# Optimization experiments

Measured on AMD Instinct MI355X. Metric: run time of the kernel, lower is better.

Reference implementation:

```python
import jax, jax.numpy as jnp
import numpy as np

T, B, L, CTX, H = 512, 512, 16, 64, 128
STATE_DIM, SHOT, PID, DATA = 32, 12, 35, 23


def setup_inputs() -> dict:
    key = jax.random.key(0)
    ks = jax.random.split(key, 64)
    k = iter(ks)
    def rn(shape, s=0.1):
        return (jax.random.normal(next(k), shape) * s).astype(jnp.float32)
    xs = jax.random.normal(next(k), (T, B, DATA), jnp.float32)
    xs = xs.at[:, :, 12].set(jax.random.randint(next(k), (T, B), 0, SHOT).astype(jnp.float32))
    xs = xs.at[:, :, 17].set(jax.random.randint(next(k), (T, B), 0, PID).astype(jnp.float32))
    xs = xs.at[:, :, 20].set(jax.random.randint(next(k), (T, B), 0, SHOT).astype(jnp.float32))
    return dict(
        total_xs=jnp.zeros((1,), jnp.float32),
        xs=xs,
        ts=jnp.linspace(0.0, 2.0, T).astype(jnp.float32),
        noise_std=jnp.asarray(0.1, jnp.float32),
        z0_noise=jax.random.normal(next(k), (B, L), jnp.float32),
        bm_noise=jax.random.normal(next(k), (T - 1, B, L), jnp.float32),
        shot_emb=rn((SHOT, 8)), player_emb=rn((PID, 8)),
        gru_wih=rn((3 * H, STATE_DIM)), gru_whh=rn((3 * H, H)),
        gru_bih=rn((3 * H,)), gru_bhh=rn((3 * H,)),
        enc_w=rn((CTX, H)), enc_b=rn((CTX,)),
        qz0_w=rn((2 * L, CTX)), qz0_b=rn((2 * L,)),
        f_w1=rn((H, L + CTX)), f_b1=rn((H,)), f_w2=rn((H, H)), f_b2=rn((H,)),
        f_w3=rn((L, H)), f_b3=rn((L,)),
        h_w1=rn((H, L)), h_b1=rn((H,)), h_w2=rn((H, H)), h_b2=rn((H,)),
        h_w3=rn((L, H)), h_b3=rn((L,)),
        g_w1=rn((L, H)), g_b1=rn((L, H)), g_w2=rn((L, H)), g_b2=rn((L,)),
        proj_w=rn((STATE_DIM, L)), proj_b=rn((STATE_DIM,)),
        pz0_mean=jnp.zeros((1, L), jnp.float32), pz0_logstd=jnp.zeros((1, L), jnp.float32),
        act_w=rn((128, L)), act_b=rn((128,)),
        act_land_w=rn((2, 128)), act_shot_w=rn((SHOT, 128)), act_move_w=rn((2, 128)),
    )


def _forward(xs, noise_std, shot_emb, player_emb, gru_wih, gru_whh, gru_bih, gru_bhh,
             enc_w, enc_b, qz0_w, qz0_b,
             f_w1, f_b1, f_w2, f_b2, f_w3, f_b3,
             h_w1, h_b1, h_w2, h_b2, h_w3, h_b3,
             g_w1, g_b1, g_w2, g_b2,
             proj_w, proj_b, pz0_mean, pz0_logstd,
             act_w, act_b, act_land_w, act_shot_w, act_move_w,
             ts, z0_noise, bm_noise):
    # --- SDE_embed_and_transform: replace shot/player id cols with embeddings ---
    state = xs[:, :, :18]
    shot_ids = state[:, :, 12].astype(jnp.int32)
    pid_ids = state[:, :, 17].astype(jnp.int32)
    state_t = jnp.concatenate([state[:, :, :12], shot_emb[shot_ids],
                               state[:, :, 13:17], player_emb[pid_ids]], axis=-1)  # (T,B,32)
    xs_t = jnp.concatenate([state_t, xs[:, :, 18:]], axis=-1)  # (T,B,37)
    # --- Encoder: GRU over time-reversed states, linear head, flip back ---
    def gru_step(h, xt):
        gi = xt @ gru_wih.T + gru_bih
        gh = h @ gru_whh.T + gru_bhh
        ir, iz, inn = jnp.split(gi, 3, axis=-1)
        hr, hz, hn = jnp.split(gh, 3, axis=-1)
        r = jax.nn.sigmoid(ir + hr)
        zg = jax.nn.sigmoid(iz + hz)
        n = jnp.tanh(inn + r * hn)
        hnew = (1.0 - zg) * n + zg * h
        return hnew, hnew
    h0 = jnp.zeros((xs.shape[1], gru_whh.shape[1]), xs.dtype)
    _, hs = jax.lax.scan(gru_step, h0, state_t[::-1])
    ctx = (hs @ enc_w.T + enc_b)[::-1]  # (T,B,CTX)
    # --- posterior z0 ---
    qm, qls = jnp.split(ctx[0] @ qz0_w.T + qz0_b, 2, axis=1)
    z0 = qm + jnp.exp(qls) * z0_noise
    # --- Euler-Maruyama with logqp; searchsorted(right) -> ctx[min(i+1,T-1)] = ctx[i+1] ---
    dts = ts[1:] - ts[:-1]  # (T-1,)
    dW = jnp.sqrt(dts)[:, None, None] * bm_noise
    ctx_steps = ctx[1:]
    def mlp3(x, w1, b1, w2, b2, w3, b3):
        h1 = jax.nn.softplus(x @ w1.T + b1)
        h2 = jax.nn.softplus(h1 @ w2.T + b2)
        return h2 @ w3.T + b3
    def g_diag(y):  # (B,L): per-latent-dim scalar nets, batched over L
        hg = jax.nn.softplus(y[:, :, None] * g_w1[None] + g_b1[None])  # (B,L,H)
        return jax.nn.sigmoid(jnp.einsum('blh,lh->bl', hg, g_w2) + g_b2)
    def sde_step(z, inp):
        c, dw, dt = inp
        f_val = mlp3(jnp.concatenate([z, c], axis=1), f_w1, f_b1, f_w2, f_b2, f_w3, f_b3)
        h_val = mlp3(z, h_w1, h_b1, h_w2, h_b2, h_w3, h_b3)
        g_val = g_diag(z)
        u = (f_val - h_val) / g_val
        logr = 0.5 * jnp.sum(u * u, axis=1) * dt
        z_new = z + f_val * dt + g_val * dw
        return z_new, (z_new, logr)
    _, (z_tail, log_ratio) = jax.lax.scan(sde_step, z0, (ctx_steps, dW, dts))
    zs = jnp.concatenate([z0[None], z_tail], axis=0)  # (T,B,L)
    _xs = zs @ proj_w.T + proj_b  # (T,B,32)
    # --- action model losses ---
    a = jax.nn.relu(zs @ act_w.T + act_b)
    land = (a @ act_land_w.T).reshape(-1, 2)
    shot_logits = (a @ act_shot_w.T).reshape(-1, act_shot_w.shape[0])
    move = (a @ act_move_w.T).reshape(-1, 2)
    true_actions = xs_t[:, :, -5:]
    true_land = true_actions[:, :, :2].reshape(-1, 2)
    true_move = true_actions[:, :, 3:].reshape(-1, 2)
    true_shot = true_actions[:, :, 2].astype(jnp.int32).reshape(-1)
    land_loss = jnp.mean((land - true_land) ** 2)
    move_loss = jnp.mean((move - true_move) ** 2)
    logp = jax.nn.log_softmax(shot_logits, axis=-1)
    picked = jnp.take_along_axis(logp, true_shot[:, None], axis=1)[:, 0]
    mask = (true_shot != 0).astype(logp.dtype)  # CrossEntropy ignore_index=0
    shot_loss = -jnp.sum(picked * mask) / jnp.maximum(jnp.sum(mask), 1.0)
    # --- reconstruction log-likelihood ---
    xs_state = xs_t[:, :, :STATE_DIM]
    LOG2PI = 1.8378770664093453
    log_pxs = jnp.mean(jnp.sum(
        -0.5 * ((xs_state - _xs) / noise_std) ** 2 - jnp.log(noise_std) - 0.5 * LOG2PI,
        axis=(0, 2)))
    # --- KL(q(z0) || p(z0)) ---
    var_q = jnp.exp(2.0 * qls)
    var_p = jnp.exp(2.0 * pz0_logstd)
    kl = pz0_logstd - qls + (var_q + (qm - pz0_mean) ** 2) / (2.0 * var_p) - 0.5
    logqp0 = jnp.mean(jnp.sum(kl, axis=1))
    logqp_path = jnp.mean(jnp.sum(log_ratio, axis=0))
    return log_pxs, logqp0 + logqp_path + land_loss + shot_loss + move_loss


def reference(total_xs, xs, ts, noise_std, z0_noise, bm_noise, shot_emb, player_emb,
              gru_wih, gru_whh, gru_bih, gru_bhh, enc_w, enc_b, qz0_w, qz0_b,
              f_w1, f_b1, f_w2, f_b2, f_w3, f_b3, h_w1, h_b1, h_w2, h_b2, h_w3, h_b3,
              g_w1, g_b1, g_w2, g_b2, proj_w, proj_b, pz0_mean, pz0_logstd,
              act_w, act_b, act_land_w, act_shot_w, act_move_w):
    return _forward(xs, noise_std, shot_emb, player_emb, gru_wih, gru_whh, gru_bih, gru_bhh,
                    enc_w, enc_b, qz0_w, qz0_b,
                    f_w1, f_b1, f_w2, f_b2, f_w3, f_b3,
                    h_w1, h_b1, h_w2, h_b2, h_w3, h_b3,
                    g_w1, g_b1, g_w2, g_b2,
                    proj_w, proj_b, pz0_mean, pz0_logstd,
                    act_w, act_b, act_land_w, act_shot_w, act_move_w,
                    ts, z0_noise, bm_noise)
```

## Files before the change

### kernel.cpp

```cpp
#include <hip/hip_runtime.h>
#include <cstdint>

typedef _Float16 f16;
typedef _Float16 f16x2 __attribute__((ext_vector_type(2)));

#define T_STEPS 512
#define B_SZ 512
#define LOG2PI 1.8378770664093453f

__device__ __forceinline__ uint32_t packh2(float a, float b) {
  f16x2 v; v[0] = (f16)a; v[1] = (f16)b;
  return __builtin_bit_cast(uint32_t, v);
}

__device__ __forceinline__ float fdot2(uint32_t a, uint32_t b, float c) {
#if defined(__AMDGCN__) && __has_builtin(__builtin_amdgcn_fdot2)
  return __builtin_amdgcn_fdot2(__builtin_bit_cast(f16x2, a),
                                __builtin_bit_cast(f16x2, b), c, false);
#else
  f16x2 x = __builtin_bit_cast(f16x2, a), y = __builtin_bit_cast(f16x2, b);
  return c + (float)x[0] * (float)y[0] + (float)x[1] * (float)y[1];
#endif
}

#define DOT4(acc, w0, w1, w2, w3, v)                                     \
  do {                                                                   \
    acc = fdot2((w0), (v).x, acc); acc = fdot2((w1), (v).y, acc);        \
    acc = fdot2((w2), (v).z, acc); acc = fdot2((w3), (v).w, acc);        \
  } while (0)

__device__ __forceinline__ float sigmoidf_(float x) {
  return 1.0f / (1.0f + __expf(-x));
}
__device__ __forceinline__ float tanhf_(float x) {
  float ax = fabsf(x);
  float t = __expf(-2.0f * ax);
  float r = (1.0f - t) / (1.0f + t);
  return copysignf(r, x);
}
__device__ __forceinline__ float softplusf_(float x) {
  return fmaxf(x, 0.0f) + __logf(1.0f + __expf(-fabsf(x)));
}

__global__ __launch_bounds__(256) void k_embed(
    const float* __restrict__ xs, const float* __restrict__ shot_emb,
    const float* __restrict__ player_emb, f16* __restrict__ state_t,
    float* __restrict__ accums) {
  if (blockIdx.x == 0 && threadIdx.x < 16) accums[threadIdx.x] = 0.0f;
  size_t idx = (size_t)blockIdx.x * 256 + threadIdx.x;
  const float* xp = xs + idx * 23;
  f16* op = state_t + idx * 32;
  int sid = (int)xp[12];
  int pid = (int)xp[17];
#pragma unroll
  for (int i = 0; i < 12; ++i) op[i] = (f16)xp[i];
  const float* se = shot_emb + sid * 8;
#pragma unroll
  for (int i = 0; i < 8; ++i) op[12 + i] = (f16)se[i];
#pragma unroll
  for (int i = 0; i < 4; ++i) op[20 + i] = (f16)xp[13 + i];
  const float* pe = player_emb + pid * 8;
#pragma unroll
  for (int i = 0; i < 8; ++i) op[24 + i] = (f16)pe[i];
}

__global__ __launch_bounds__(448, 4) void k_gru(
    const f16* __restrict__ state_t, const float* __restrict__ wih,
    const float* __restrict__ whh, const float* __restrict__ bih,
    const float* __restrict__ bhh, const float* __restrict__ enc_w,
    const float* __restrict__ enc_b, const float* __restrict__ qz0_w,
    const float* __restrict__ qz0_b, const float* __restrict__ z0_noise,
    const float* __restrict__ pz0_mean, const float* __restrict__ pz0_logstd,
    f16* __restrict__ ctx, float* __restrict__ z0_out,
    float* __restrict__ accums) {
  __shared__ __align__(16) uint32_t s_x[16];
  __shared__ __align__(16) uint32_t s_h[64];
  __shared__ float s_gi[384], s_gh[384];
  __shared__ float s_ctx0[64];
  __shared__ float s_q[32];

  const int tid = threadIdx.x;
  const int bg = blockIdx.x;
  const uint32_t* stu = (const uint32_t*)state_t;

  uint32_t wA[64];
  uint32_t wB[16];
  float bi = 0.f, bh = 0.f, encbr = 0.f;

  if (tid < 384) {
    const float* whr = whh + (size_t)tid * 128;
#pragma unroll
    for (int i = 0; i < 64; ++i) wA[i] = packh2(whr[2 * i], whr[2 * i + 1]);
    const float* wxr = wih + (size_t)tid * 32;
#pragma unroll
    for (int i = 0; i < 16; ++i) wB[i] = packh2(wxr[2 * i], wxr[2 * i + 1]);
    bi = bih[tid];
    bh = bhh[tid];
  } else {
    int cc = tid - 384;
    const float* wer = enc_w + (size_t)cc * 128;
#pragma unroll
    for (int i = 0; i < 64; ++i) wA[i] = packh2(wer[2 * i], wer[2 * i + 1]);
    encbr = enc_b[cc];
  }

  if (tid < 64) s_h[tid] = 0u;
  if (tid < 4)
    *(uint4*)&s_x[tid * 4] =
        *(const uint4*)(stu + ((size_t)(T_STEPS - 1) * B_SZ + bg) * 16 + tid * 4);
  float h_old = 0.0f;
  __syncthreads();

  for (int t = T_STEPS - 1; t >= 0; --t) {
    uint4 xpref = make_uint4(0, 0, 0, 0);
    if (tid >= 128 && tid < 132 && t > 0)
      xpref = *(const uint4*)(stu + ((size_t)(t - 1) * B_SZ + bg) * 16 +
                              (tid - 128) * 4);
    if (tid < 384) {
      float ax0 = bi, ax1 = 0.f;
      const uint4* xq = (const uint4*)s_x;
#pragma unroll
      for (int j = 0; j < 4; ++j) {
        uint4 v = xq[j];
        if (j & 1) { DOT4(ax1, wB[4 * j], wB[4 * j + 1], wB[4 * j + 2], wB[4 * j + 3], v); }
        else       { DOT4(ax0, wB[4 * j], wB[4 * j + 1], wB[4 * j + 2], wB[4 * j + 3], v); }
      }
      float ah0 = bh, ah1 = 0.f;
      const uint4* hq = (const uint4*)s_h;
#pragma unroll
      for (int j = 0; j < 16; ++j) {
        uint4 v = hq[j];
        if (j & 1) { DOT4(ah1, wA[4 * j], wA[4 * j + 1], wA[4 * j + 2], wA[4 * j + 3], v); }
        else       { DOT4(ah0, wA[4 * j], wA[4 * j + 1], wA[4 * j + 2], wA[4 * j + 3], v); }
      }
      s_gi[tid] = ax0 + ax1;
      s_gh[tid] = ah0 + ah1;
    } else if (t < T_STEPS - 1) {
      int cc = tid - 384;
      float a0 = encbr, a1 = 0.f;
      const uint4* hq = (const uint4*)s_h;
#pragma unroll
      for (int j = 0; j < 16; ++j) {
        uint4 v = hq[j];
        if (j & 1) { DOT4(a1, wA[4 * j], wA[4 * j + 1], wA[4 * j + 2], wA[4 * j + 3], v); }
        else       { DOT4(a0, wA[4 * j], wA[4 * j + 1], wA[4 * j + 2], wA[4 * j + 3], v); }
      }
      ctx[((size_t)(t + 1) * B_SZ + bg) * 64 + cc] = (f16)(a0 + a1);
    }
    __syncthreads();
    if (tid < 128) {
      float r = sigmoidf_(s_gi[tid] + s_gh[tid]);
      float zg = sigmoidf_(s_gi[128 + tid] + s_gh[128 + tid]);
      float n = tanhf_(s_gi[256 + tid] + r * s_gh[256 + tid]);
      float hnew = (1.0f - zg) * n + zg * h_old;
      h_old = hnew;
      ((f16*)s_h)[tid] = (f16)hnew;
    } else if (tid >= 128 && tid < 132 && t > 0) {
      *(uint4*)&s_x[(tid - 128) * 4] = xpref;
    }
    __syncthreads();
  }

  if (tid >= 384) {
    int cc = tid - 384;
    float a0 = encbr, a1 = 0.f;
    const uint4* hq = (const uint4*)s_h;
#pragma unroll
    for (int j = 0; j < 16; ++j) {
      uint4 v = hq[j];
      if (j & 1) { DOT4(a1, wA[4 * j], wA[4 * j + 1], wA[4 * j + 2], wA[4 * j + 3], v); }
      else       { DOT4(a0, wA[4 * j], wA[4 * j + 1], wA[4 * j + 2], wA[4 * j + 3], v); }
    }
    float val = a0 + a1;
    ctx[(size_t)bg * 64 + cc] = (f16)val;
    s_ctx0[cc] = val;
  }
  __syncthreads();
  if (tid < 32) {
    float acc = qz0_b[tid];
#pragma unroll 8
    for (int k = 0; k < 64; ++k) acc += qz0_w[tid * 64 + k] * s_ctx0[k];
    s_q[tid] = acc;
  }
  __syncthreads();
  if (tid < 16) {
    float qm = s_q[tid], qls = s_q[16 + tid];
    float z0v = qm + __expf(qls) * z0_noise[bg * 16 + tid];
    z0_out[bg * 16 + tid] = z0v;
    float pm = pz0_mean[tid], pls = pz0_logstd[tid];
    float var_q = __expf(2.0f * qls);
    float var_p = __expf(2.0f * pls);
    float dm = qm - pm;
    float kl = pls - qls + (var_q + dm * dm) / (2.0f * var_p) - 0.5f;
    atomicAdd(&accums[5], kl);
  }
}

__global__ __launch_bounds__(256, 2) void k_sde(
    const f16* __restrict__ ctx, const float* __restrict__ z0_in,
    const float* __restrict__ ts, const float* __restrict__ bm_noise,
    const float* __restrict__ fw1, const float* __restrict__ fb1,
    const float* __restrict__ fw2, const float* __restrict__ fb2,
    const float* __restrict__ fw3, const float* __restrict__ fb3,
    const float* __restrict__ hw1, const float* __restrict__ hb1,
    const float* __restrict__ hw2, const float* __restrict__ hb2,
    const float* __restrict__ hw3, const float* __restrict__ hb3,
    const float* __restrict__ gw1, const float* __restrict__ gb1,
    const float* __restrict__ gw2, const float* __restrict__ gb2,
    f16* __restrict__ zs, float* __restrict__ accums) {
  __shared__ __align__(16) uint32_t s_x2[40];
  __shared__ __align__(16) uint32_t s_h1f[64];
  __shared__ __align__(16) uint32_t s_h1h[64];
  __shared__ __align__(16) uint32_t s_h2[2][64];
  __shared__ float s_zf[16];
  __shared__ __align__(16) float s_gp[128];
  __shared__ __align__(16) float s_p3[256];
  __shared__ float s_dts[T_STEPS];

  const int tid = threadIdx.x;
  const int bg = blockIdx.x;

  uint32_t uw[56];
  uint32_t wP2[64];
  uint32_t wP3[8];
  float bias1r = 0.f, bias2r = 0.f, gb2r = 0.f, fb3r = 0.f, hb3r = 0.f;

  if (tid < 128) {
    const float* w = fw1 + (size_t)tid * 80;
#pragma unroll
    for (int i = 0; i < 40; ++i) uw[i] = packh2(w[2 * i], w[2 * i + 1]);
    bias1r = fb1[tid];
  } else {
    int u = tid - 128;
    const float* w = hw1 + (size_t)u * 16;
#pragma unroll
    for (int i = 0; i < 8; ++i) uw[i] = packh2(w[2 * i], w[2 * i + 1]);
    bias1r = hb1[u];
    int l = u & 15, k8 = u >> 4;
#pragma unroll
    for (int i = 0; i < 16; ++i) {
      int h = k8 * 16 + i;
      uw[8 + i] = __builtin_bit_cast(uint32_t, gw1[l * 128 + h]);
      uw[24 + i] = __builtin_bit_cast(uint32_t, gb1[l * 128 + h]);
      uw[40 + i] = __builtin_bit_cast(uint32_t, gw2[l * 128 + h]);
    }
  }
  {
    int mlp = tid >> 7, u = tid & 127;
    const float* w = (mlp ? hw2 : fw2) + (size_t)u * 128;
#pragma unroll
    for (int i = 0; i < 64; ++i) wP2[i] = packh2(w[2 * i], w[2 * i + 1]);
    bias2r = (mlp ? hb2 : fb2)[u];
  }
  {
    int mlp = tid >> 7, o = tid & 15, k8 = (tid >> 4) & 7;
    const float* w = (mlp ? hw3 : fw3) + (size_t)o * 128 + k8 * 16;
#pragma unroll
    for (int i = 0; i < 8; ++i) wP3[i] = packh2(w[2 * i], w[2 * i + 1]);
  }
  if (tid < 16) {
    fb3r = fb3[tid];
    hb3r = hb3[tid];
    gb2r = gb2[tid];
  }
  for (int i = tid; i < T_STEPS - 1; i += 256) s_dts[i] = ts[i + 1] - ts[i];

  if (tid < 16) {
    float z = z0_in[bg * 16 + tid];
    s_zf[tid] = z;
    ((f16*)s_x2)[tid] = (f16)z;
    zs[(size_t)bg * 16 + tid] = (f16)z;
  }
  if (tid >= 16 && tid < 24) {
    int q = tid - 16;
    *(uint4*)&s_x2[8 + q * 4] =
        *(const uint4*)((const uint32_t*)ctx + ((size_t)1 * B_SZ + bg) * 32 + q * 4);
  }
  float path_acc = 0.0f;
  __syncthreads();

  for (int t = 0; t < T_STEPS - 1; ++t) {
    float bm_cur = 0.f;
    uint4 cpref = make_uint4(0, 0, 0, 0);
    if (tid < 16) bm_cur = bm_noise[((size_t)t * B_SZ + bg) * 16 + tid];
    if (tid >= 16 && tid < 24 && t <= T_STEPS - 3) {
      int q = tid - 16;
      cpref = *(const uint4*)((const uint32_t*)ctx +
                              ((size_t)(t + 2) * B_SZ + bg) * 32 + q * 4);
    }
    if (tid < 128) {
      float a0 = bias1r, a1 = 0.f;
      const uint4* xq = (const uint4*)s_x2;
#pragma unroll
      for (int j = 0; j < 10; ++j) {
        uint4 v = xq[j];
        if (j & 1) { DOT4(a1, uw[4 * j], uw[4 * j + 1], uw[4 * j + 2], uw[4 * j + 3], v); }
        else       { DOT4(a0, uw[4 * j], uw[4 * j + 1], uw[4 * j + 2], uw[4 * j + 3], v); }
      }
      ((f16*)s_h1f)[tid] = (f16)softplusf_(a0 + a1);
    } else {
      int u = tid - 128;
      const uint4* zq = (const uint4*)s_x2;
      float a0 = bias1r, a1 = 0.f;
      uint4 v0 = zq[0], v1 = zq[1];
      DOT4(a0, uw[0], uw[1], uw[2], uw[3], v0);
      DOT4(a1, uw[4], uw[5], uw[6], uw[7], v1);
      ((f16*)s_h1h)[u] = (f16)softplusf_(a0 + a1);
      int l = u & 15, k8 = u >> 4;
      float y = s_zf[l];
      float acc = 0.f;
#pragma unroll
      for (int i = 0; i < 16; ++i) {
        float pre = fmaf(y, __builtin_bit_cast(float, uw[8 + i]),
                         __builtin_bit_cast(float, uw[24 + i]));
        acc = fmaf(softplusf_(pre), __builtin_bit_cast(float, uw[40 + i]), acc);
      }
      s_gp[l * 8 + k8] = acc;
    }
    __syncthreads();
    {
      const uint4* hq = (const uint4*)((tid >> 7) ? s_h1h : s_h1f);
      float a0 = bias2r, a1 = 0.f, a2 = 0.f, a3 = 0.f;
#pragma unroll
      for (int j = 0; j < 16; j += 4) {
        uint4 v0 = hq[j], v1 = hq[j + 1], v2 = hq[j + 2], v3 = hq[j + 3];
        DOT4(a0, wP2[4 * j], wP2[4 * j + 1], wP2[4 * j + 2], wP2[4 * j + 3], v0);
        DOT4(a1, wP2[4 * j + 4], wP2[4 * j + 5], wP2[4 * j + 6], wP2[4 * j + 7], v1);
        DOT4(a2, wP2[4 * j + 8], wP2[4 * j + 9], wP2[4 * j + 10], wP2[4 * j + 11], v2);
        DOT4(a3, wP2[4 * j + 12], wP2[4 * j + 13], wP2[4 * j + 14], wP2[4 * j + 15], v3);
      }
      ((f16*)s_h2[tid >> 7])[tid & 127] = (f16)softplusf_((a0 + a1) + (a2 + a3));
    }
    __syncthreads();
    {
      int mlp = tid >> 7, o = tid & 15, k8 = (tid >> 4) & 7;
      const uint4* hq = (const uint4*)&s_h2[mlp][k8 * 8];
      uint4 v0 = hq[0], v1 = hq[1];
      float a0 = 0.f, a1 = 0.f;
      DOT4(a0, wP3[0], wP3[1], wP3[2], wP3[3], v0);
      DOT4(a1, wP3[4], wP3[5], wP3[6], wP3[7], v1);
      s_p3[(mlp * 16 + o) * 8 + k8] = a0 + a1;
    }
    __syncthreads();
    if (tid < 16) {
      int l = tid;
      const float4* fp = (const float4*)&s_p3[l * 8];
      const float4* hp = (const float4*)&s_p3[(16 + l) * 8];
      const float4* gp = (const float4*)&s_gp[l * 8];
      float4 f0 = fp[0], f1v = fp[1], h0 = hp[0], h1v = hp[1];
      float4 g0 = gp[0], g1 = gp[1];
      float fv = fb3r + ((f0.x + f0.y) + (f0.z + f0.w)) +
                 ((f1v.x + f1v.y) + (f1v.z + f1v.w));
      float hv = hb3r + ((h0.x + h0.y) + (h0.z + h0.w)) +
                 ((h1v.x + h1v.y) + (h1v.z + h1v.w));
      float gv = sigmoidf_(gb2r + ((g0.x + g0.y) + (g0.z + g0.w)) +
                           ((g1.x + g1.y) + (g1.z + g1.w)));
      float dt = s_dts[t];
      float u = (fv - hv) / gv;
      float lsum = u * u;
      lsum += __shfl_xor(lsum, 1);
      lsum += __shfl_xor(lsum, 2);
      lsum += __shfl_xor(lsum, 4);
      lsum += __shfl_xor(lsum, 8);
      if (l == 0) path_acc += 0.5f * lsum * dt;
      float zn = s_zf[l] + fv * dt + gv * (sqrtf(dt) * bm_cur);
      s_zf[l] = zn;
      ((f16*)s_x2)[l] = (f16)zn;
      zs[((size_t)(t + 1) * B_SZ + bg) * 16 + l] = (f16)zn;
    } else if (tid >= 16 && tid < 24 && t <= T_STEPS - 3) {
      int q = tid - 16;
      *(uint4*)&s_x2[8 + q * 4] = cpref;
    }
    __syncthreads();
  }
  if (tid == 0) atomicAdd(&accums[6], path_acc);
}

__global__ __launch_bounds__(256) void k_dec(
    const f16* __restrict__ zs, const f16* __restrict__ state_t,
    const float* __restrict__ xs, const float* __restrict__ proj_w,
    const float* __restrict__ proj_b, const float* __restrict__ act_w,
    const float* __restrict__ act_b, const float* __restrict__ land_w,
    const float* __restrict__ shot_w, const float* __restrict__ move_w,
    float* __restrict__ accums) {
  __shared__ __align__(16) uint32_t s_proj[32 * 8];
  __shared__ __align__(16) uint32_t s_act[128 * 8];
  __shared__ __align__(16) uint32_t s_head[128 * 8];
  __shared__ float s_pb[32], s_ab[128];
  __shared__ float s_red[4 * 5];

  const int tid = threadIdx.x;
  if (tid < 256) {
    int i = tid >> 3, kp = tid & 7;
    s_proj[tid] = packh2(proj_w[i * 16 + 2 * kp], proj_w[i * 16 + 2 * kp + 1]);
  }
  for (int id = tid; id < 1024; id += 256) {
    int j = id >> 3, kp = id & 7;
    s_act[id] = packh2(act_w[j * 16 + 2 * kp], act_w[j * 16 + 2 * kp + 1]);
  }
  for (int id = tid; id < 1024; id += 256) {
    int j = id >> 3, p = id & 7;
    int h0 = 2 * p, h1 = 2 * p + 1;
    float w0 = (h0 < 2) ? land_w[h0 * 128 + j]
                        : (h0 < 14 ? shot_w[(h0 - 2) * 128 + j]
                                   : move_w[(h0 - 14) * 128 + j]);
    float w1 = (h1 < 2) ? land_w[h1 * 128 + j]
                        : (h1 < 14 ? shot_w[(h1 - 2) * 128 + j]
                                   : move_w[(h1 - 14) * 128 + j]);
    s_head[j * 8 + p] = packh2(w0, w1);
  }
  if (tid < 32) s_pb[tid] = proj_b[tid];
  if (tid < 128) s_ab[tid] = act_b[tid];
  __syncthreads();

  size_t idx0 = (size_t)blockIdx.x * 512 + tid;
  size_t idx1 = idx0 + 256;
  uint32_t zA[8], zB[8];
  {
    const uint4* za = (const uint4*)(zs + idx0 * 16);
    const uint4* zb = (const uint4*)(zs + idx1 * 16);
    uint4 a0 = za[0], a1 = za[1], b0 = zb[0], b1 = zb[1];
    zA[0] = a0.x; zA[1] = a0.y; zA[2] = a0.z; zA[3] = a0.w;
    zA[4] = a1.x; zA[5] = a1.y; zA[6] = a1.z; zA[7] = a1.w;
    zB[0] = b0.x; zB[1] = b0.y; zB[2] = b0.z; zB[3] = b0.w;
    zB[4] = b1.x; zB[5] = b1.y; zB[6] = b1.z; zB[7] = b1.w;
  }
  uint32_t stA[16], stB[16];
  {
// ... 118 lines not shown

extern "C" void kernel_launch(void* const* d_in, const int* in_sizes, int n_in,
                              void* d_out, int out_size, void* d_ws,
                              size_t ws_size, hipStream_t stream) {
  const float* xs = (const float*)d_in[1];
  const float* ts = (const float*)d_in[2];
  const float* noise_std = (const float*)d_in[3];
  const float* z0_noise = (const float*)d_in[4];
  const float* bm_noise = (const float*)d_in[5];
  const float* shot_emb = (const float*)d_in[6];
  const float* player_emb = (const float*)d_in[7];
  const float* gru_wih = (const float*)d_in[8];
  const float* gru_whh = (const float*)d_in[9];
  const float* gru_bih = (const float*)d_in[10];
  const float* gru_bhh = (const float*)d_in[11];
  const float* enc_w = (const float*)d_in[12];
  const float* enc_b = (const float*)d_in[13];
  const float* qz0_w = (const float*)d_in[14];
  const float* qz0_b = (const float*)d_in[15];
  const float* f_w1 = (const float*)d_in[16];
  const float* f_b1 = (const float*)d_in[17];
  const float* f_w2 = (const float*)d_in[18];
  const float* f_b2 = (const float*)d_in[19];
  const float* f_w3 = (const float*)d_in[20];
  const float* f_b3 = (const float*)d_in[21];
  const float* h_w1 = (const float*)d_in[22];
  const float* h_b1 = (const float*)d_in[23];
  const float* h_w2 = (const float*)d_in[24];
  const float* h_b2 = (const float*)d_in[25];
  const float* h_w3 = (const float*)d_in[26];
  const float* h_b3 = (const float*)d_in[27];
  const float* g_w1 = (const float*)d_in[28];
  const float* g_b1 = (const float*)d_in[29];
  const float* g_w2 = (const float*)d_in[30];
  const float* g_b2 = (const float*)d_in[31];
  const float* proj_w = (const float*)d_in[32];
  const float* proj_b = (const float*)d_in[33];
  const float* pz0_mean = (const float*)d_in[34];
  const float* pz0_logstd = (const float*)d_in[35];
  const float* act_w = (const float*)d_in[36];
  const float* act_b = (const float*)d_in[37];
  const float* act_land_w = (const float*)d_in[38];
  const float* act_shot_w = (const float*)d_in[39];
  const float* act_move_w = (const float*)d_in[40];

  char* ws = (char*)d_ws;
  float* accums = (float*)ws;
  f16* state_t = (f16*)(ws + 256);
  f16* ctx = (f16*)(ws + 256 + 16777216);
  float* z0b = (float*)(ws + 256 + 16777216 + 33554432);
  f16* zs = (f16*)(ws + 256 + 16777216 + 33554432 + 32768);

  k_embed<<<1024, 256, 0, stream>>>(xs, shot_emb, player_emb, state_t, accums);
  k_gru<<<512, 448, 0, stream>>>(state_t, gru_wih, gru_whh, gru_bih, gru_bhh,
                                 enc_w, enc_b, qz0_w, qz0_b, z0_noise, pz0_mean,
                                 pz0_logstd, ctx, z0b, accums);
  k_sde<<<512, 256, 0, stream>>>(ctx, z0b, ts, bm_noise, f_w1, f_b1, f_w2, f_b2,
                                 f_w3, f_b3, h_w1, h_b1, h_w2, h_b2, h_w3, h_b3,
                                 g_w1, g_b1, g_w2, g_b2, zs, accums);
  k_dec<<<512, 256, 0, stream>>>(zs, state_t, xs, proj_w, proj_b, act_w, act_b,
                                 act_land_w, act_shot_w, act_move_w, accums);
  k_fin<<<1, 64, 0, stream>>>(accums, noise_std, (float*)d_out);
}
```

Before: 2.005 ms.

## Restructure GRU and SDE recurrences to cut barriers per timestep

The GRU kernel now uses 256 threads. Each hidden unit's three gate dot products are split across two half-waves and combined with a lane shuffle, so the shared gate buffers and one barrier per step are gone. The SDE kernel is reorganised by wavefront: drift MLP, prior MLP, diffusion and context projection run in separate waves. The context part of the first layer is precomputed one step ahead, and per-step barriers drop from four to two. Trajectories are buffered in LDS and written out at the end, at the cost of much higher register pressure (w2 holds 128 regs) and less thread parallelism per step.

```diff
diff --git a/kernel.cpp b/kernel.cpp
--- a/kernel.cpp
+++ b/kernel.cpp
@@ -7,6 +7,8 @@
 #define T_STEPS 512
 #define B_SZ 512
 #define LOG2PI 1.8378770664093453f
+
+#define BAR_LDS() asm volatile("s_waitcnt lgkmcnt(0)\n\ts_barrier" ::: "memory")
 
 __device__ __forceinline__ uint32_t packh2(float a, float b) {
   f16x2 v; v[0] = (f16)a; v[1] = (f16)b;
@@ -64,7 +66,7 @@
   for (int i = 0; i < 8; ++i) op[24 + i] = (f16)pe[i];
 }
 
-__global__ __launch_bounds__(448, 4) void k_gru(
+__global__ __launch_bounds__(256, 2) void k_gru(
     const f16* __restrict__ state_t, const float* __restrict__ wih,
     const float* __restrict__ whh, const float* __restrict__ bih,
     const float* __restrict__ bhh, const float* __restrict__ enc_w,
@@ -73,107 +75,147 @@
     const float* __restrict__ pz0_mean, const float* __restrict__ pz0_logstd,
     f16* __restrict__ ctx, float* __restrict__ z0_out,
     float* __restrict__ accums) {
-  __shared__ __align__(16) uint32_t s_x[16];
-  __shared__ __align__(16) uint32_t s_h[64];
-  __shared__ float s_gi[384], s_gh[384];
+  __shared__ __align__(16) f16 s_hbuf[2][128];
   __shared__ float s_ctx0[64];
   __shared__ float s_q[32];
 
   const int tid = threadIdx.x;
   const int bg = blockIdx.x;
+  const int lane = tid & 63;
+  const int wid = tid >> 6;
+  const int l31 = lane & 31;
+  const int kh = lane >> 5;
+  const int d = wid * 32 + l31;
+  const int e = wid * 16 + (lane & 15);
+  const int eh = (lane >> 4) & 1;
   const uint32_t* stu = (const uint32_t*)state_t;
 
-  uint32_t wA[64];
-  uint32_t wB[16];
-  float bi = 0.f, bh = 0.f, encbr = 0.f;
-
-  if (tid < 384) {
-    const float* whr = whh + (size_t)tid * 128;
-#pragma unroll
-    for (int i = 0; i < 64; ++i) wA[i] = packh2(whr[2 * i], whr[2 * i + 1]);
-    const float* wxr = wih + (size_t)tid * 32;
-#pragma unroll
-    for (int i = 0; i < 16; ++i) wB[i] = packh2(wxr[2 * i], wxr[2 * i + 1]);
-    bi = bih[tid];
-    bh = bhh[tid];
+  uint32_t wR[32], wZ[32], wN[32];
+  uint32_t wXR[16], wXZ[16], wXN[16];
+  uint32_t wE[32];
+  float bR = 0.f, bZ = 0.f, bIN = 0.f, bHN = 0.f, encbr = 0.f;
+
+  {
+    const float* r = whh + (size_t)d * 128 + kh * 64;
+#pragma unroll
+    for (int i = 0; i < 32; ++i) wR[i] = packh2(r[2 * i], r[2 * i + 1]);
+    r = whh + (size_t)(128 + d) * 128 + kh * 64;
+#pragma unroll
+    for (int i = 0; i < 32; ++i) wZ[i] = packh2(r[2 * i], r[2 * i + 1]);
+    r = whh + (size_t)(256 + d) * 128 + kh * 64;
+#pragma unroll
+    for (int i = 0; i < 32; ++i) wN[i] = packh2(r[2 * i], r[2 * i + 1]);
+  }
+  if (kh == 0) {
+    const float* r = wih + (size_t)d * 32;
+#pragma unroll
+    for (int i = 0; i < 16; ++i) wXR[i] = packh2(r[2 * i], r[2 * i + 1]);
+    r = wih + (size_t)(128 + d) * 32;
+#pragma unroll
+    for (int i = 0; i < 16; ++i) wXZ[i] = packh2(r[2 * i], r[2 * i + 1]);
+    r = wih + (size_t)(256 + d) * 32;
+#pragma unroll
+    for (int i = 0; i < 16; ++i) wXN[i] = packh2(r[2 * i], r[2 * i + 1]);
+    bR = bih[d] + bhh[d];
+    bZ = bih[128 + d] + bhh[128 + d];
+    bIN = bih[256 + d];
+    bHN = bhh[256 + d];
   } else {
-    int cc = tid - 384;
-    const float* wer = enc_w + (size_t)cc * 128;
-#pragma unroll
-    for (int i = 0; i < 64; ++i) wA[i] = packh2(wer[2 * i], wer[2 * i + 1]);
-    encbr = enc_b[cc];
-  }
-
-  if (tid < 64) s_h[tid] = 0u;
-  if (tid < 4)
-    *(uint4*)&s_x[tid * 4] =
-        *(const uint4*)(stu + ((size_t)(T_STEPS - 1) * B_SZ + bg) * 16 + tid * 4);
+    const float* r = enc_w + (size_t)e * 128 + eh * 64;
+#pragma unroll
+    for (int i = 0; i < 32; ++i) wE[i] = packh2(r[2 * i], r[2 * i + 1]);
+    encbr = enc_b[e];
+  }
+
+  if (tid < 128) s_hbuf[0][tid] = (f16)0.0f;
   float h_old = 0.0f;
   __syncthreads();
 
+  int cur = 0;
+  uint4 xc0, xc1, xc2, xc3;
+  {
+    const uint4* xr = (const uint4*)(stu + ((size_t)(T_STEPS - 1) * B_SZ + bg) * 16);
+    xc0 = xr[0]; xc1 = xr[1]; xc2 = xr[2]; xc3 = xr[3];
+  }
+
   for (int t = T_STEPS - 1; t >= 0; --t) {
-    uint4 xpref = make_uint4(0, 0, 0, 0);
-    if (tid >= 128 && tid < 132 && t > 0)
-      xpref = *(const uint4*)(stu + ((size_t)(t - 1) * B_SZ + bg) * 16 +
-                              (tid - 128) * 4);
-    if (tid < 384) {
-      float ax0 = bi, ax1 = 0.f;
-      const uint4* xq = (const uint4*)s_x;
-#pragma unroll
-      for (int j = 0; j < 4; ++j) {
-        uint4 v = xq[j];
-        if (j & 1) { DOT4(ax1, wB[4 * j], wB[4 * j + 1], wB[4 * j + 2], wB[4 * j + 3], v); }
-        else       { DOT4(ax0, wB[4 * j], wB[4 * j + 1], wB[4 * j + 2], wB[4 * j + 3], v); }
-      }
-      float ah0 = bh, ah1 = 0.f;
-      const uint4* hq = (const uint4*)s_h;
-#pragma unroll
-      for (int j = 0; j < 16; ++j) {
+    uint4 xn0, xn1, xn2, xn3;
+    if (t > 0) {
+      const uint4* xr = (const uint4*)(stu + ((size_t)(t - 1) * B_SZ + bg) * 16);
+      xn0 = xr[0]; xn1 = xr[1]; xn2 = xr[2]; xn3 = xr[3];
+    }
+    float aR = 0.f, aZ = 0.f, aIN = 0.f, aHN = 0.f;
+    {
+      const uint4* hq = (const uint4*)&s_hbuf[cur][kh * 64];
+#pragma unroll
+      for (int j = 0; j < 8; ++j) {
         uint4 v = hq[j];
-        if (j & 1) { DOT4(ah1, wA[4 * j], wA[4 * j + 1], wA[4 * j + 2], wA[4 * j + 3], v); }
-        else       { DOT4(ah0, wA[4 * j], wA[4 * j + 1], wA[4 * j + 2], wA[4 * j + 3], v); }
-      }
-      s_gi[tid] = ax0 + ax1;
-      s_gh[tid] = ah0 + ah1;
+        DOT4(aR, wR[4 * j], wR[4 * j + 1], wR[4 * j + 2], wR[4 * j + 3], v);
+        DOT4(aZ, wZ[4 * j], wZ[4 * j + 1], wZ[4 * j + 2], wZ[4 * j + 3], v);
+        DOT4(aHN, wN[4 * j], wN[4 * j + 1], wN[4 * j + 2], wN[4 * j + 3], v);
+      }
+    }
+    float enc0 = 0.f, enc1 = 0.f;
+    if (kh == 0) {
+      DOT4(aR, wXR[0], wXR[1], wXR[2], wXR[3], xc0);
+      DOT4(aR, wXR[4], wXR[5], wXR[6], wXR[7], xc1);
+      DOT4(aR, wXR[8], wXR[9], wXR[10], wXR[11], xc2);
+      DOT4(aR, wXR[12], wXR[13], wXR[14], wXR[15], xc3);
+      DOT4(aZ, wXZ[0], wXZ[1], wXZ[2], wXZ[3], xc0);
+      DOT4(aZ, wXZ[4], wXZ[5], wXZ[6], wXZ[7], xc1);
+      DOT4(aZ, wXZ[8], wXZ[9], wXZ[10], wXZ[11], xc2);
+      DOT4(aZ, wXZ[12], wXZ[13], wXZ[14], wXZ[15], xc3);
+      DOT4(aIN, wXN[0], wXN[1], wXN[2], wXN[3], xc0);
+      DOT4(aIN, wXN[4], wXN[5], wXN[6], wXN[7], xc1);
+      DOT4(aIN, wXN[8], wXN[9], wXN[10], wXN[11], xc2);
+      DOT4(aIN, wXN[12], wXN[13], wXN[14], wXN[15], xc3);
+      aR += bR; aZ += bZ; aIN += bIN; aHN += bHN;
     } else if (t < T_STEPS - 1) {
-      int cc = tid - 384;
-      float a0 = encbr, a1 = 0.f;
-      const uint4* hq = (const uint4*)s_h;
-#pragma unroll
-      for (int j = 0; j < 16; ++j) {
-        uint4 v = hq[j];
-        if (j & 1) { DOT4(a1, wA[4 * j], wA[4 * j + 1], wA[4 * j + 2], wA[4 * j + 3], v); }
-        else       { DOT4(a0, wA[4 * j], wA[4 * j + 1], wA[4 * j + 2], wA[4 * j + 3], v); }
-      }
-      ctx[((size_t)(t + 1) * B_SZ + bg) * 64 + cc] = (f16)(a0 + a1);
-    }
-    __syncthreads();
-    if (tid < 128) {
-      float r = sigmoidf_(s_gi[tid] + s_gh[tid]);
-      float zg = sigmoidf_(s_gi[128 + tid] + s_gh[128 + tid]);
-      float n = tanhf_(s_gi[256 + tid] + r * s_gh[256 + tid]);
+      const uint4* hq2 = (const uint4*)&s_hbuf[cur][eh * 64];
+#pragma unroll
+      for (int j = 0; j < 8; ++j) {
+        uint4 v = hq2[j];
+        if (j & 1) { DOT4(enc1, wE[4 * j], wE[4 * j + 1], wE[4 * j + 2], wE[4 * j + 3], v); }
+        else       { DOT4(enc0, wE[4 * j], wE[4 * j + 1], wE[4 * j + 2], wE[4 * j + 3], v); }
+      }
+    }
+    aR += __shfl_xor(aR, 32);
+    aZ += __shfl_xor(aZ, 32);
+    aHN += __shfl_xor(aHN, 32);
+    if (kh == 0) {
+      float r = sigmoidf_(aR);
+      float zg = sigmoidf_(aZ);
+      float n = tanhf_(aIN + r * aHN);
       float hnew = (1.0f - zg) * n + zg * h_old;
       h_old = hnew;
-      ((f16*)s_h)[tid] = (f16)hnew;
-    } else if (tid >= 128 && tid < 132 && t > 0) {
-      *(uint4*)&s_x[(tid - 128) * 4] = xpref;
-    }
-    __syncthreads();
-  }
-
-  if (tid >= 384) {
-    int cc = tid - 384;
-    float a0 = encbr, a1 = 0.f;
-    const uint4* hq = (const uint4*)s_h;
-#pragma unroll
-    for (int j = 0; j < 16; ++j) {
-      uint4 v = hq[j];
-      if (j & 1) { DOT4(a1, wA[4 * j], wA[4 * j + 1], wA[4 * j + 2], wA[4 * j + 3], v); }
-      else       { DOT4(a0, wA[4 * j], wA[4 * j + 1], wA[4 * j + 2], wA[4 * j + 3], v); }
-    }
-    float val = a0 + a1;
-    ctx[(size_t)bg * 64 + cc] = (f16)val;
-    s_ctx0[cc] = val;
+      s_hbuf[cur ^ 1][d] = (f16)hnew;
+    } else if (t < T_STEPS - 1) {
+      float es = enc0 + enc1;
+      es += __shfl_xor(es, 16);
+      if (eh == 0)
+        ctx[((size_t)(t + 1) * B_SZ + bg) * 64 + e] = (f16)(es + encbr);
+    }
+    BAR_LDS();
+    cur ^= 1;
+    if (t > 0) { xc0 = xn0; xc1 = xn1; xc2 = xn2; xc3 = xn3; }
+  }
+
+  if (kh == 1) {
+    float e0 = 0.f, e1 = 0.f;
+    const uint4* hq2 = (const uint4*)&s_hbuf[cur][eh * 64];
+#pragma unroll
+    for (int j = 0; j < 8; ++j) {
+      uint4 v = hq2[j];
+      if (j & 1) { DOT4(e1, wE[4 * j], wE[4 * j + 1], wE[4 * j + 2], wE[4 * j + 3], v); }
+      else       { DOT4(e0, wE[4 * j], wE[4 * j + 1], wE[4 * j + 2], wE[4 * j + 3], v); }
+    }
+    float es = e0 + e1;
+    es += __shfl_xor(es, 16);
+    if (eh == 0) {
+      float val = es + encbr;
+      ctx[(size_t)bg * 64 + e] = (f16)val;
+      s_ctx0[e] = val;
+    }
   }
   __syncthreads();
   if (tid < 32) {
@@ -208,172 +250,292 @@
     const float* __restrict__ gw1, const float* __restrict__ gb1,
     const float* __restrict__ gw2, const float* __restrict__ gb2,
     f16* __restrict__ zs, float* __restrict__ accums) {
-  __shared__ __align__(16) uint32_t s_x2[40];
-  __shared__ __align__(16) uint32_t s_h1f[64];
-  __shared__ __align__(16) uint32_t s_h1h[64];
-  __shared__ __align__(16) uint32_t s_h2[2][64];
+  __shared__ __align__(16) uint32_t s_x2z[8];
   __shared__ float s_zf[16];
-  __shared__ __align__(16) float s_gp[128];
-  __shared__ __align__(16) float s_p3[256];
+  __shared__ __align__(16) uint32_t s_h1f[64], s_h2f[64];
+  __shared__ __align__(16) uint32_t s_h1h[64], s_h2h[64];
+  __shared__ __align__(16) float s_pctx[2][128];
+  __shared__ float s_v3h[16];
+  __shared__ float s_gp[2][16];
   __shared__ float s_dts[T_STEPS];
+  __shared__ __align__(16) f16 s_zbuf[T_STEPS * 16];
 
   const int tid = threadIdx.x;
   const int bg = blockIdx.x;
-
-  uint32_t uw[56];
-  uint32_t wP2[64];
-  uint32_t wP3[8];
-  float bias1r = 0.f, bias2r = 0.f, gb2r = 0.f, fb3r = 0.f, hb3r = 0.f;
-
-  if (tid < 128) {
-    const float* w = fw1 + (size_t)tid * 80;
-#pragma unroll
-    for (int i = 0; i < 40; ++i) uw[i] = packh2(w[2 * i], w[2 * i + 1]);
-    bias1r = fb1[tid];
+  const int lane = tid & 63;
+  const int wid = tid >> 6;
+
+  uint32_t w1[16];
+  uint32_t w2[128];
+  uint32_t w3[16];
+  uint32_t wcx[64];
+  float gw1v[16], gb1v[16], gw2v[16];
+  float b1a = 0.f, b1b = 0.f, b2a = 0.f, b2b = 0.f, b3r = 0.f, gb2r = 0.f;
+
+  if (wid == 0) {
+    const float* r0 = fw1 + (size_t)(2 * lane) * 80;
+    const float* r1 = fw1 + (size_t)(2 * lane + 1) * 80;
+#pragma unroll
+    for (int i = 0; i < 8; ++i) {
+      w1[i] = packh2(r0[2 * i], r0[2 * i + 1]);
+      w1[8 + i] = packh2(r1[2 * i], r1[2 * i + 1]);
+    }
+    b1a = fb1[2 * lane]; b1b = fb1[2 * lane + 1];
+    r0 = fw2 + (size_t)(2 * lane) * 128;
+    r1 = fw2 + (size_t)(2 * lane + 1) * 128;
+#pragma unroll
+    for (int i = 0; i < 64; ++i) {
+      w2[i] = packh2(r0[2 * i], r0[2 * i + 1]);
+      w2[64 + i] = packh2(r1[2 * i], r1[2 * i + 1]);
+    }
+    b2a = fb2[2 * lane]; b2b = fb2[2 * lane + 1];
+    {
+      int o = lane & 15, q = lane >> 4;
+      const float* r3 = fw3 + (size_t)o * 128 + q * 32;
+#pragma unroll
+      for (int i = 0; i < 16; ++i) w3[i] = packh2(r3[2 * i], r3[2 * i + 1]);
+      b3r = fb3[o];
+      gb2r = gb2[o];
+    }
+  } else if (wid == 1) {
+    const float* r0 = hw1 + (size_t)(2 * lane) * 16;
+    const float* r1 = hw1 + (size_t)(2 * lane + 1) * 16;
+#pragma unroll
+    for (int i = 0; i < 8; ++i) {
+      w1[i] = packh2(r0[2 * i], r0[2 * i + 1]);
+      w1[8 + i] = packh2(r1[2 * i], r1[2 * i + 1]);
+    }
+    b1a = hb1[2 * lane]; b1b = hb1[2 * lane + 1];
+    r0 = hw2 + (size_t)(2 * lane) * 128;
+    r1 = hw2 + (size_t)(2 * lane + 1) * 128;
+#pragma unroll
+    for (int i = 0; i < 64; ++i) {
+      w2[i] = packh2(r0[2 * i], r0[2 * i + 1]);
+      w2[64 + i] = packh2(r1[2 * i], r1[2 * i + 1]);
+    }
+    b2a = hb2[2 * lane]; b2b = hb2[2 * lane + 1];
+    {
+      int o = lane & 15, q = lane >> 4;
+      const float* r3 = hw3 + (size_t)o * 128 + q * 32;
+#pragma unroll
+      for (int i = 0; i < 16; ++i) w3[i] = packh2(r3[2 * i], r3[2 * i + 1]);
+      b3r = hb3[o];
+    }
   } else {
-    int u = tid - 128;
-    const float* w = hw1 + (size_t)u * 16;
-#pragma unroll
-    for (int i = 0; i < 8; ++i) uw[i] = packh2(w[2 * i], w[2 * i + 1]);
-    bias1r = hb1[u];
-    int l = u & 15, k8 = u >> 4;
-#pragma unroll
-    for (int i = 0; i < 16; ++i) {
-      int h = k8 * 16 + i;
-      uw[8 + i] = __builtin_bit_cast(uint32_t, gw1[l * 128 + h]);
-      uw[24 + i] = __builtin_bit_cast(uint32_t, gb1[l * 128 + h]);
-      uw[40 + i] = __builtin_bit_cast(uint32_t, gw2[l * 128 + h]);
-    }
-  }
-  {
-    int mlp = tid >> 7, u = tid & 127;
-    const float* w = (mlp ? hw2 : fw2) + (size_t)u * 128;
-#pragma unroll
-    for (int i = 0; i < 64; ++i) wP2[i] = packh2(w[2 * i], w[2 * i + 1]);
-    bias2r = (mlp ? hb2 : fb2)[u];
-  }
-  {
-    int mlp = tid >> 7, o = tid & 15, k8 = (tid >> 4) & 7;
-    const float* w = (mlp ? hw3 : fw3) + (size_t)o * 128 + k8 * 16;
-#pragma unroll
-    for (int i = 0; i < 8; ++i) wP3[i] = packh2(w[2 * i], w[2 * i + 1]);
-  }
-  if (tid < 16) {
-    fb3r = fb3[tid];
-    hb3r = hb3[tid];
-    gb2r = gb2[tid];
+    int l = lane & 15, q = lane >> 4;
+    int hbase = (wid - 2) * 64 + q * 16;
+#pragma unroll
+    for (int j = 0; j < 16; ++j) {
+      int h = hbase + j;
+      gw1v[j] = gw1[l * 128 + h];
+      gb1v[j] = gb1[l * 128 + h];
+      gw2v[j] = gw2[l * 128 + h];
+    }
+    if (wid == 3) {
+      const float* r0 = fw1 + (size_t)(2 * lane) * 80 + 16;
+      const float* r1 = fw1 + (size_t)(2 * lane + 1) * 80 + 16;
+#pragma unroll
+      for (int i = 0; i < 32; ++i) {
+        wcx[i] = packh2(r0[2 * i], r0[2 * i + 1]);
+        wcx[32 + i] = packh2(r1[2 * i], r1[2 * i + 1]);
+      }
+    }
   }
   for (int i = tid; i < T_STEPS - 1; i += 256) s_dts[i] = ts[i + 1] - ts[i];
 
   if (tid < 16) {
     float z = z0_in[bg * 16 + tid];
     s_zf[tid] = z;
-    ((f16*)s_x2)[tid] = (f16)z;
-    zs[(size_t)bg * 16 + tid] = (f16)z;
-  }
-  if (tid >= 16 && tid < 24) {
-    int q = tid - 16;
-    *(uint4*)&s_x2[8 + q * 4] =
-        *(const uint4*)((const uint32_t*)ctx + ((size_t)1 * B_SZ + bg) * 32 + q * 4);
+    s_zbuf[tid] = (f16)z;
+  }
+  if (tid < 8)
+    s_x2z[tid] = packh2(z0_in[bg * 16 + 2 * tid], z0_in[bg * 16 + 2 * tid + 1]);
+  float bm_cur = 0.f;
+  if (wid == 0 && lane < 16)
+    bm_cur = bm_noise[((size_t)0 * B_SZ + bg) * 16 + lane];
+
+  uint4 cc[8];
+  if (wid == 3) {
+    const uint4* cr =
+        (const uint4*)((const uint32_t*)ctx + ((size_t)1 * B_SZ + bg) * 32);
+    uint4 a0 = cr[0], a1 = cr[1], a2 = cr[2], a3 = cr[3];
+    uint4 a4 = cr[4], a5 = cr[5], a6 = cr[6], a7 = cr[7];
+    float p0 = 0.f, p0b = 0.f, p1 = 0.f, p1b = 0.f;
+    DOT4(p0, wcx[0], wcx[1], wcx[2], wcx[3], a0);
+    DOT4(p0b, wcx[4], wcx[5], wcx[6], wcx[7], a1);
+    DOT4(p0, wcx[8], wcx[9], wcx[10], wcx[11], a2);
+    DOT4(p0b, wcx[12], wcx[13], wcx[14], wcx[15], a3);
+    DOT4(p0, wcx[16], wcx[17], wcx[18], wcx[19], a4);
+    DOT4(p0b, wcx[20], wcx[21], wcx[22], wcx[23], a5);
+    DOT4(p0, wcx[24], wcx[25], wcx[26], wcx[27], a6);
+    DOT4(p0b, wcx[28], wcx[29], wcx[30], wcx[31], a7);
+    DOT4(p1, wcx[32], wcx[33], wcx[34], wcx[35], a0);
+    DOT4(p1b, wcx[36], wcx[37], wcx[38], wcx[39], a1);
+    DOT4(p1, wcx[40], wcx[41], wcx[42], wcx[43], a2);
+    DOT4(p1b, wcx[44], wcx[45], wcx[46], wcx[47], a3);
+    DOT4(p1, wcx[48], wcx[49], wcx[50], wcx[51], a4);
+    DOT4(p1b, wcx[52], wcx[53], wcx[54], wcx[55], a5);
+    DOT4(p1, wcx[56], wcx[57], wcx[58], wcx[59], a6);
+    DOT4(p1b, wcx[60], wcx[61], wcx[62], wcx[63], a7);
+    *(float2*)&s_pctx[0][2 * lane] = make_float2(p0 + p0b, p1 + p1b);
+    const uint4* c2 =
+        (const uint4*)((const uint32_t*)ctx + ((size_t)2 * B_SZ + bg) * 32);
+#pragma unroll
+    for (int i = 0; i < 8; ++i) cc[i] = c2[i];
   }
   float path_acc = 0.0f;
+  float fv_r = 0.0f;
   __syncthreads();
 
   for (int t = 0; t < T_STEPS - 1; ++t) {
-    float bm_cur = 0.f;
-    uint4 cpref = make_uint4(0, 0, 0, 0);
-    if (tid < 16) bm_cur = bm_noise[((size_t)t * B_SZ + bg) * 16 + tid];
-    if (tid >= 16 && tid < 24 && t <= T_STEPS - 3) {
-      int q = tid - 16;
-      cpref = *(const uint4*)((const uint32_t*)ctx +
-                              ((size_t)(t + 2) * B_SZ + bg) * 32 + q * 4);
-    }
-    if (tid < 128) {
-      float a0 = bias1r, a1 = 0.f;
-      const uint4* xq = (const uint4*)s_x2;
-#pragma unroll
-      for (int j = 0; j < 10; ++j) {
-        uint4 v = xq[j];
-        if (j & 1) { DOT4(a1, uw[4 * j], uw[4 * j + 1], uw[4 * j + 2], uw[4 * j + 3], v); }
-        else       { DOT4(a0, uw[4 * j], uw[4 * j + 1], uw[4 * j + 2], uw[4 * j + 3], v); }
-      }
-      ((f16*)s_h1f)[tid] = (f16)softplusf_(a0 + a1);
+    if (wid == 0) {
+      const uint4* zq = (const uint4*)s_x2z;
+      uint4 zv0 = zq[0], zv1 = zq[1];
+      float2 pc = *(const float2*)&s_pctx[t & 1][2 * lane];
+      float a0 = b1a + pc.x, a1 = b1b + pc.y;
+      DOT4(a0, w1[0], w1[1], w1[2], w1[3], zv0);
+      DOT4(a0, w1[4], w1[5], w1[6], w1[7], zv1);
+      DOT4(a1, w1[8], w1[9], w1[10], w1[11], zv0);
+      DOT4(a1, w1[12], w1[13], w1[14], w1[15], zv1);
+      s_h1f[lane] = packh2(softplusf_(a0), softplusf_(a1));
+      const uint4* hq = (const uint4*)s_h1f;
+      float c0 = b2a, c0b = 0.f, c1 = b2b, c1b = 0.f;
+#pragma unroll
+      for (int j = 0; j < 16; ++j) {
+        uint4 v = hq[j];
+        if (j & 1) {
+          DOT4(c0b, w2[4 * j], w2[4 * j + 1], w2[4 * j + 2], w2[4 * j + 3], v);
+          DOT4(c1b, w2[64 + 4 * j], w2[65 + 4 * j], w2[66 + 4 * j], w2[67 + 4 * j], v);
+        } else {
+          DOT4(c0, w2[4 * j], w2[4 * j + 1], w2[4 * j + 2], w2[4 * j + 3], v);
+          DOT4(c1, w2[64 + 4 * j], w2[65 + 4 * j], w2[66 + 4 * j], w2[67 + 4 * j], v);
+        }
+      }
+      s_h2f[lane] = packh2(softplusf_(c0 + c0b), softplusf_(c1 + c1b));
+      {
+        int q = lane >> 4;
+        const uint4* h2q = (const uint4*)&s_h2f[q * 16];
+        uint4 v0 = h2q[0], v1 = h2q[1], v2 = h2q[2], v3 = h2q[3];
+        float f3 = 0.f, f3b = 0.f;
+        DOT4(f3, w3[0], w3[1], w3[2], w3[3], v0);
+        DOT4(f3b, w3[4], w3[5], w3[6], w3[7], v1);
+        DOT4(f3, w3[8], w3[9], w3[10], w3[11], v2);
+        DOT4(f3b, w3[12], w3[13], w3[14], w3[15], v3);
+        f3 += f3b;
+        f3 += __shfl_xor(f3, 16);
+        f3 += __shfl_xor(f3, 32);
+        fv_r = f3 + b3r;
+      }
+    } else if (wid == 1) {
+      const uint4* zq = (const uint4*)s_x2z;
+      uint4 zv0 = zq[0], zv1 = zq[1];
+      float a0 = b1a, a1 = b1b;
+      DOT4(a0, w1[0], w1[1], w1[2], w1[3], zv0);
+      DOT4(a0, w1[4], w1[5], w1[6], w1[7], zv1);
+      DOT4(a1, w1[8], w1[9], w1[10], w1[11], zv0);
+      DOT4(a1, w1[12], w1[13], w1[14], w1[15], zv1);
+      s_h1h[lane] = packh2(softplusf_(a0), softplusf_(a1));
+      const uint4* hq = (const uint4*)s_h1h;
+      float c0 = b2a, c0b = 0.f, c1 = b2b, c1b = 0.f;
+#pragma unroll
+      for (int j = 0; j < 16; ++j) {
+        uint4 v = hq[j];
+        if (j & 1) {
+          DOT4(c0b, w2[4 * j], w2[4 * j + 1], w2[4 * j + 2], w2[4 * j + 3], v);
+          DOT4(c1b, w2[64 + 4 * j], w2[65 + 4 * j], w2[66 + 4 * j], w2[67 + 4 * j], v);
+        } else {
+          DOT4(c0, w2[4 * j], w2[4 * j + 1], w2[4 * j + 2], w2[4 * j + 3], v);
+          DOT4(c1, w2[64 + 4 * j], w2[65 + 4 * j], w2[66 + 4 * j], w2[67 + 4 * j], v);
+        }
+      }
+      s_h2h[lane] = packh2(softplusf_(c0 + c0b), softplusf_(c1 + c1b));
+      {
+        int q = lane >> 4;
+        const uint4* h2q = (const uint4*)&s_h2h[q * 16];
+        uint4 v0 = h2q[0], v1 = h2q[1], v2 = h2q[2], v3 = h2q[3];
+        float h3 = 0.f, h3b = 0.f;
+        DOT4(h3, w3[0], w3[1], w3[2], w3[3], v0);
+        DOT4(h3b, w3[4], w3[5], w3[6], w3[7], v1);
+        DOT4(h3, w3[8], w3[9], w3[10], w3[11], v2);
+        DOT4(h3b, w3[12], w3[13], w3[14], w3[15], v3);
+        h3 += h3b;
+        h3 += __shfl_xor(h3, 16);
+        h3 += __shfl_xor(h3, 32);
+        if (lane < 16) s_v3h[lane] = h3 + b3r;
+      }
     } else {
-      int u = tid - 128;
-      const uint4* zq = (const uint4*)s_x2;
-      float a0 = bias1r, a1 = 0.f;
-      uint4 v0 = zq[0], v1 = zq[1];
-      DOT4(a0, uw[0], uw[1], uw[2], uw[3], v0);
-      DOT4(a1, uw[4], uw[5], uw[6], uw[7], v1);
-      ((f16*)s_h1h)[u] = (f16)softplusf_(a0 + a1);
-      int l = u & 15, k8 = u >> 4;
+      int l = lane & 15;
       float y = s_zf[l];
       float acc = 0.f;
 #pragma unroll
-      for (int i = 0; i < 16; ++i) {
-        float pre = fmaf(y, __builtin_bit_cast(float, uw[8 + i]),
-                         __builtin_bit_cast(float, uw[24 + i]));
-        acc = fmaf(softplusf_(pre), __builtin_bit_cast(float, uw[40 + i]), acc);
-      }
-      s_gp[l * 8 + k8] = acc;
-    }
-    __syncthreads();
-    {
-      const uint4* hq = (const uint4*)((tid >> 7) ? s_h1h : s_h1f);
-      float a0 = bias2r, a1 = 0.f, a2 = 0.f, a3 = 0.f;
-#pragma unroll
-      for (int j = 0; j < 16; j += 4) {
-        uint4 v0 = hq[j], v1 = hq[j + 1], v2 = hq[j + 2], v3 = hq[j + 3];
-        DOT4(a0, wP2[4 * j], wP2[4 * j + 1], wP2[4 * j + 2], wP2[4 * j + 3], v0);
-        DOT4(a1, wP2[4 * j + 4], wP2[4 * j + 5], wP2[4 * j + 6], wP2[4 * j + 7], v1);
-        DOT4(a2, wP2[4 * j + 8], wP2[4 * j + 9], wP2[4 * j + 10], wP2[4 * j + 11], v2);
-        DOT4(a3, wP2[4 * j + 12], wP2[4 * j + 13], wP2[4 * j + 14], wP2[4 * j + 15], v3);
-      }
-      ((f16*)s_h2[tid >> 7])[tid & 127] = (f16)softplusf_((a0 + a1) + (a2 + a3));
-    }
-    __syncthreads();
-    {
-      int mlp = tid >> 7, o = tid & 15, k8 = (tid >> 4) & 7;
-      const uint4* hq = (const uint4*)&s_h2[mlp][k8 * 8];
-      uint4 v0 = hq[0], v1 = hq[1];
-      float a0 = 0.f, a1 = 0.f;
-      DOT4(a0, wP3[0], wP3[1], wP3[2], wP3[3], v0);
-      DOT4(a1, wP3[4], wP3[5], wP3[6], wP3[7], v1);
-      s_p3[(mlp * 16 + o) * 8 + k8] = a0 + a1;
-    }
-    __syncthreads();
-    if (tid < 16) {
-      int l = tid;
-      const float4* fp = (const float4*)&s_p3[l * 8];
-      const float4* hp = (const float4*)&s_p3[(16 + l) * 8];
-      const float4* gp = (const float4*)&s_gp[l * 8];
-      float4 f0 = fp[0], f1v = fp[1], h0 = hp[0], h1v = hp[1];
-      float4 g0 = gp[0], g1 = gp[1];
-      float fv = fb3r + ((f0.x + f0.y) + (f0.z + f0.w)) +
-                 ((f1v.x + f1v.y) + (f1v.z + f1v.w));
-      float hv = hb3r + ((h0.x + h0.y) + (h0.z + h0.w)) +
-                 ((h1v.x + h1v.y) + (h1v.z + h1v.w));
-      float gv = sigmoidf_(gb2r + ((g0.x + g0.y) + (g0.z + g0.w)) +
-                           ((g1.x + g1.y) + (g1.z + g1.w)));
+      for (int j = 0; j < 16; ++j) {
+        float pre = fmaf(y, gw1v[j], gb1v[j]);
+        acc = fmaf(softplusf_(pre), gw2v[j], acc);
+      }
+      acc += __shfl_xor(acc, 16);
+      acc += __shfl_xor(acc, 32);
+      if (lane < 16) s_gp[wid - 2][l] = acc;
+      if (wid == 3) {
+        if (t <= T_STEPS - 3) {
+          float p0 = 0.f, p0b = 0.f, p1 = 0.f, p1b = 0.f;
+          DOT4(p0, wcx[0], wcx[1], wcx[2], wcx[3], cc[0]);
+          DOT4(p0b, wcx[4], wcx[5], wcx[6], wcx[7], cc[1]);
+          DOT4(p0, wcx[8], wcx[9], wcx[10], wcx[11], cc[2]);
+          DOT4(p0b, wcx[12], wcx[13], wcx[14], wcx[15], cc[3]);
+          DOT4(p0, wcx[16], wcx[17], wcx[18], wcx[19], cc[4]);
+          DOT4(p0b, wcx[20], wcx[21], wcx[22], wcx[23], cc[5]);
+          DOT4(p0, wcx[24], wcx[25], wcx[26], wcx[27], cc[6]);
+          DOT4(p0b, wcx[28], wcx[29], wcx[30], wcx[31], cc[7]);
+          DOT4(p1, wcx[32], wcx[33], wcx[34], wcx[35], cc[0]);
+          DOT4(p1b, wcx[36], wcx[37], wcx[38], wcx[39], cc[1]);
+          DOT4(p1, wcx[40], wcx[41], wcx[42], wcx[43], cc[2]);
+          DOT4(p1b, wcx[44], wcx[45], wcx[46], wcx[47], cc[3]);
+          DOT4(p1, wcx[48], wcx[49], wcx[50], wcx[51], cc[4]);
+          DOT4(p1b, wcx[52], wcx[53], wcx[54], wcx[55], cc[5]);
+          DOT4(p1, wcx[56], wcx[57], wcx[58], wcx[59], cc[6]);
+          DOT4(p1b, wcx[60], wcx[61], wcx[62], wcx[63], cc[7]);
+          *(float2*)&s_pctx[(t + 1) & 1][2 * lane] =
+              make_float2(p0 + p0b, p1 + p1b);
+        }
+        if (t <= T_STEPS - 4) {
+          const uint4* cr = (const uint4*)((const uint32_t*)ctx +
+                                           ((size_t)(t + 3) * B_SZ + bg) * 32);
+#pragma unroll
+          for (int i = 0; i < 8; ++i) cc[i] = cr[i];
+        }
+      }
+    }
+    BAR_LDS();
+    if (wid == 0 && lane < 16) {
+      int l = lane;
+      float hv = s_v3h[l];
+      float gv = sigmoidf_(gb2r + s_gp[0][l] + s_gp[1][l]);
       float dt = s_dts[t];
-      float u = (fv - hv) / gv;
-      float lsum = u * u;
+      float uu = (fv_r - hv) / gv;
+      float lsum = uu * uu;
       lsum += __shfl_xor(lsum, 1);
       lsum += __shfl_xor(lsum, 2);
       lsum += __shfl_xor(lsum, 4);
       lsum += __shfl_xor(lsum, 8);
       if (l == 0) path_acc += 0.5f * lsum * dt;
-      float zn = s_zf[l] + fv * dt + gv * (sqrtf(dt) * bm_cur);
+      float zn = s_zf[l] + fv_r * dt + gv * (sqrtf(dt) * bm_cur);
       s_zf[l] = zn;
-      ((f16*)s_x2)[l] = (f16)zn;
-      zs[((size_t)(t + 1) * B_SZ + bg) * 16 + l] = (f16)zn;
-    } else if (tid >= 16 && tid < 24 && t <= T_STEPS - 3) {
-      int q = tid - 16;
-      *(uint4*)&s_x2[8 + q * 4] = cpref;
-    }
-    __syncthreads();
-  }
-  if (tid == 0) atomicAdd(&accums[6], path_acc);
+      s_zbuf[(t + 1) * 16 + l] = (f16)zn;
+      float zo = __shfl_xor(zn, 1);
+      if (!(l & 1)) s_x2z[l >> 1] = packh2(zn, zo);
+      if (t < T_STEPS - 2)
+        bm_cur = bm_noise[((size_t)(t + 1) * B_SZ + bg) * 16 + l];
+    }
+    BAR_LDS();
+  }
+  if (wid == 0 && lane == 0) atomicAdd(&accums[6], path_acc);
+#pragma unroll
+  for (int it = 0; it < 4; ++it) {
+    int idx = it * 256 + tid;
+    int row = idx >> 1, half = idx & 1;
+    uint4 v = *(const uint4*)((const uint32_t*)s_zbuf + row * 8 + half * 4);
+    *(uint4*)((uint32_t*)zs + ((size_t)row * B_SZ + bg) * 8 + half * 4) = v;
+  }
 }
 
 __global__ __launch_bounds__(256) void k_dec(
@@ -598,7 +760,7 @@
   f16* zs = (f16*)(ws + 256 + 16777216 + 33554432 + 32768);
 
   k_embed<<<1024, 256, 0, stream>>>(xs, shot_emb, player_emb, state_t, accums);
-  k_gru<<<512, 448, 0, stream>>>(state_t, gru_wih, gru_whh, gru_bih, gru_bhh,
+  k_gru<<<512, 256, 0, stream>>>(state_t, gru_wih, gru_whh, gru_bih, gru_bhh,
                                  enc_w, enc_b, qz0_w, qz0_b, z0_noise, pz0_mean,
                                  pz0_logstd, ctx, z0b, accums);
   k_sde<<<512, 256, 0, stream>>>(ctx, z0b, ts, bm_noise, f_w1, f_b1, f_w2, f_b2,
```

After: 6.055 ms. 202% more time.
